# Optimization experiments

Measured on AMD Instinct MI355X. Metric: run time of the kernel, lower is better.

## Reference

```python
import jax, jax.numpy as jnp
import numpy as np

N = 20000      # nodes
E = 320000     # edges
IN = 300       # input_channel
HID = 100      # hidden_channel (= heads*out_channels with heads=1)
R = 50         # num_relations
B = 8          # num_bases (the 4th positional arg 'heads'=8 lands on num_bases in PyG RGATConv)
HEADS = 1
CLS = 3
Q = 64         # number of query (aspect) nodes
EPS = 1e-16


def setup_inputs() -> dict:
    key = jax.random.key(0)
    ks = jax.random.split(key, 16)
    x = jax.random.normal(ks[0], (N, IN), jnp.float32)
    edge_index = jax.random.randint(ks[1], (2, E), 0, N)
    edge_type = jax.random.randint(ks[2], (E,), 0, R)
    query_indices = jax.random.randint(ks[3], (Q,), 0, N)

    def w(k, shape, scale):
        return jax.random.normal(k, shape, jnp.float32) * scale

    comp1 = w(ks[4], (R, B), 0.3)
    basis1 = w(ks[5], (B, IN, HEADS * HID), 1.0 / np.sqrt(IN))
    q1 = w(ks[6], (HEADS * HID, HEADS), 0.1)
    k1 = w(ks[7], (HEADS * HID, HEADS), 0.1)
    b1 = jnp.zeros((HEADS * HID,), jnp.float32)
    comp2 = w(ks[8], (R, B), 0.3)
    basis2 = w(ks[9], (B, HID, HEADS * HID), 1.0 / np.sqrt(HID))
    q2 = w(ks[10], (HEADS * HID, HEADS), 0.1)
    k2 = w(ks[11], (HEADS * HID, HEADS), 0.1)
    b2 = jnp.zeros((HEADS * HID,), jnp.float32)
    Wl = w(ks[12], (CLS, HID), 1.0 / np.sqrt(HID))
    bl = jnp.zeros((CLS,), jnp.float32)
    return dict(x=x, edge_index=edge_index, edge_type=edge_type,
                query_indices=query_indices,
                comp1=comp1, basis1=basis1, q1=q1, k1=k1, b1=b1,
                comp2=comp2, basis2=basis2, q2=q2, k2=k2, b2=b2,
                Wl=Wl, bl=bl)


def segment_softmax(alpha, seg, num_segments):
    # numerically-stable softmax over edges grouped by destination node
    m = jax.ops.segment_max(alpha, seg, num_segments=num_segments)  # [N, H]
    e = jnp.exp(alpha - m[seg])
    s = jax.ops.segment_sum(e, seg, num_segments=num_segments)
    return e / (s[seg] + EPS)


def rgat_conv(x, edge_index, edge_type, comp, basis, q, k, b):
    # basis-decomposed per-relation weight: [R, in, H*out]
    W = jnp.einsum('rb,bio->rio', comp, basis)
    # transform every node under every relation once, then gather per edge
    xt = jnp.einsum('ni,rio->nro', x, W)          # [N, R, H*out]
    src, dst = edge_index[0], edge_index[1]        # j -> i (source_to_target)
    xi = xt[dst, edge_type]                        # [E, H*out]
    xj = xt[src, edge_type]                        # [E, H*out]
    qi = xi @ q                                    # [E, H]
    kj = xj @ k                                    # [E, H]
    alpha = jax.nn.leaky_relu(qi + kj, 0.2)        # additive self-attention
    alpha = segment_softmax(alpha, dst, N)         # across-relation softmax
    msg = xj.reshape(E, HEADS, HID) * alpha[:, :, None]
    out = jax.ops.segment_sum(msg, dst, num_segments=N)  # [N, H, out]
    return out.reshape(N, HEADS * HID) + b         # concat=True


def reference(x, edge_index, edge_type, query_indices,
              comp1, basis1, q1, k1, b1,
              comp2, basis2, q2, k2, b2, Wl, bl):
    h = jax.nn.relu(rgat_conv(x, edge_index, edge_type, comp1, basis1, q1, k1, b1))
    h = jax.nn.relu(rgat_conv(h, edge_index, edge_type, comp2, basis2, q2, k2, b2))
    pooled = h[query_indices].mean(axis=0)          # [HID]
    return pooled @ Wl.T + bl                       # [CLS]
```

## Files before the change

kernel.cpp:

```cpp
#include <hip/hip_runtime.h>
#include <math.h>

#define N_NODES 20000
#define E_EDGES 320000
#define IN_CH   300
#define HID     100
#define R_REL   50
#define NB      8
#define CLS     3
#define NQ      64
#define OUTW    800
#define ZW      100
#define SCAN_BLKS ((N_NODES + 255) / 256)

typedef unsigned short ushort_t;
typedef __attribute__((ext_vector_type(8))) short     short8;
typedef __attribute__((ext_vector_type(8))) unsigned short ushort8;
typedef __attribute__((ext_vector_type(4))) float     f32x4;
typedef __attribute__((ext_vector_type(2))) float     f32x2;

__device__ __forceinline__ ushort_t f2bf_rne(float f) {
    unsigned u = __float_as_uint(f);
    unsigned r = (u + 0x7fffu + ((u >> 16) & 1u)) >> 16;
    return (ushort_t)r;
}
__device__ __forceinline__ float bf2f(ushort_t u) {
    return __uint_as_float((unsigned)u << 16);
}

__global__ __launch_bounds__(256) void zero_deg2(int* __restrict__ dd,
                                                 int* __restrict__ ds) {
    int i = blockIdx.x * 256 + threadIdx.x;
    if (i < N_NODES) { dd[i] = 0; ds[i] = 0; }
}

__global__ __launch_bounds__(256) void hist2_kernel(
        const int* __restrict__ ei, int* __restrict__ dd,
        int* __restrict__ ds) {
    int e = blockIdx.x * 256 + threadIdx.x;
    if (e < E_EDGES) {
        atomicAdd(&dd[ei[E_EDGES + e]], 1);
        atomicAdd(&ds[ei[e]], 1);
    }
}

__global__ __launch_bounds__(256) void scan1_kernel(
        const int* __restrict__ deg, int* __restrict__ rowptr,
        int* __restrict__ bsum) {
    __shared__ int s[256];
    int tid = threadIdx.x;
    int idx = blockIdx.x * 256 + tid;
    int v = (idx < N_NODES) ? deg[idx] : 0;
    s[tid] = v; __syncthreads();
    #pragma unroll
    for (int off = 1; off < 256; off <<= 1) {
        int t = (tid >= off) ? s[tid - off] : 0;
        __syncthreads();
        s[tid] += t;
        __syncthreads();
    }
    if (idx < N_NODES) rowptr[idx] = s[tid] - v;
    if (tid == 255) bsum[blockIdx.x] = s[255];
}

__global__ __launch_bounds__(128) void scan2_kernel(int* __restrict__ bsum,
                                                    int* __restrict__ rowptr) {
    __shared__ int s[128];
    int tid = threadIdx.x;
    int v = (tid < SCAN_BLKS) ? bsum[tid] : 0;
    s[tid] = v; __syncthreads();
    #pragma unroll
    for (int off = 1; off < 128; off <<= 1) {
        int t = (tid >= off) ? s[tid - off] : 0;
        __syncthreads();
        s[tid] += t;
        __syncthreads();
    }
    if (tid < SCAN_BLKS) bsum[tid] = s[tid] - v;
    if (tid == 0) rowptr[N_NODES] = E_EDGES;
}

__global__ __launch_bounds__(256) void scan3_kernel(
        int* __restrict__ rowptr, const int* __restrict__ bsum,
        int* __restrict__ cursor) {
    int idx = blockIdx.x * 256 + threadIdx.x;
    if (idx < N_NODES) {
        int v = rowptr[idx] + bsum[blockIdx.x];
        rowptr[idx] = v;
        cursor[idx] = v;
    }
}

__global__ __launch_bounds__(256) void scatter_both(
        const int* __restrict__ ei, const int* __restrict__ et,
        int* __restrict__ cur_d, int* __restrict__ cur_s,
        int* __restrict__ skey, int* __restrict__ skey_s) {
    int e = blockIdx.x * 256 + threadIdx.x;
    if (e >= E_EDGES) return;
    int s = ei[e], d = ei[E_EDGES + e], rt = et[e];
    int p = atomicAdd(&cur_d[d], 1);
    skey[p] = (s << 6) | rt;
    int qp = atomicAdd(&cur_s[s], 1);
    skey_s[qp] = (p << 6) | rt;
}

__global__ __launch_bounds__(256) void split_bt_kernel(
        const float* __restrict__ basis, ushort_t* __restrict__ Bt,
        int K, int Kp) {
    int idx = blockIdx.x * 256 + threadIdx.x;
    if (idx >= OUTW * Kp) return;
    int n = idx / Kp, k = idx - n * Kp;
    int b = n / HID, o = n - b * HID;
    float v = 0.f;
    if (k < K) v = basis[((size_t)b * K + k) * HID + o];
    Bt[idx] = f2bf_rne(v);
}

#define BM 64
#define BN 160
__global__ __launch_bounds__(256) void gemm_mfma(
        const float* __restrict__ A, const ushort_t* __restrict__ Bt,
        ushort_t* __restrict__ xbh, int M, int K, int Kp, int do_relu) {
    __shared__ ushort_t As[BM][32];
    __shared__ ushort_t Bs[BN][32];
    int tid  = threadIdx.x;
    int lane = tid & 63, wave = tid >> 6;
    int ml = lane & 15, quad = lane >> 4;
    int wr = (wave >> 1) * 32, wc = (wave & 1) * 80;
    int row0 = blockIdx.y * BM, col0 = blockIdx.x * BN;
    int ra = tid >> 2, ch_a = tid & 3;
    int gr_a = row0 + ra;
    f32x4 acc[2][5] = {};
    int ksteps = Kp >> 5;
    for (int ks = 0; ks < ksteps; ks++) {
        int k0 = ks << 5;
        __syncthreads();
        {
            float vals[8];
            int kb = k0 + ch_a * 8;
            if (gr_a < M) {
                const float* ar = A + (size_t)gr_a * K;
                if (kb + 8 <= K) {
                    float4 f0 = *(const float4*)&ar[kb];
                    float4 f1 = *(const float4*)&ar[kb + 4];
                    vals[0]=f0.x; vals[1]=f0.y; vals[2]=f0.z; vals[3]=f0.w;
                    vals[4]=f1.x; vals[5]=f1.y; vals[6]=f1.z; vals[7]=f1.w;
                } else {
                    #pragma unroll
                    for (int i = 0; i < 8; i++)
                        vals[i] = (kb + i < K) ? ar[kb + i] : 0.f;
                }
                if (do_relu)
                    #pragma unroll
                    for (int i = 0; i < 8; i++) vals[i] = fmaxf(vals[i], 0.f);
            } else {
                #pragma unroll
                for (int i = 0; i < 8; i++) vals[i] = 0.f;
            }
            ushort8 hv;
            #pragma unroll
            for (int i = 0; i < 8; i++) hv[i] = f2bf_rne(vals[i]);
            int p1 = ch_a ^ (ra & 3);
            *(ushort8*)&As[ra][p1 * 8] = hv;
        }
        for (int t = tid; t < 640; t += 256) {
            int rb = t >> 2, ch = t & 3;
            int ph = ch ^ (rb & 3);
            ushort8 vh = *(const ushort8*)&Bt[(size_t)(col0 + rb) * Kp + k0 + ch * 8];
            *(ushort8*)&Bs[rb][ph * 8] = vh;
        }
        __syncthreads();
        int pq = quad ^ (ml & 3);
        short8 af[2], bf[5];
        #pragma unroll
        for (int mt = 0; mt < 2; mt++)
            af[mt] = *(const short8*)&As[wr + mt * 16 + ml][pq * 8];
        #pragma unroll
        for (int nt = 0; nt < 5; nt++)
            bf[nt] = *(const short8*)&Bs[wc + nt * 16 + ml][pq * 8];
        #pragma unroll
        for (int mt = 0; mt < 2; mt++)
            #pragma unroll
            for (int nt = 0; nt < 5; nt++)
                acc[mt][nt] = __builtin_amdgcn_mfma_f32_16x16x32_bf16(af[mt], bf[nt], acc[mt][nt], 0, 0, 0);
    }
    #pragma unroll
    for (int mt = 0; mt < 2; mt++) {
        #pragma unroll
        for (int nt = 0; nt < 5; nt++) {
            #pragma unroll
            for (int r = 0; r < 4; r++) {
                int grow = row0 + wr + mt * 16 + quad * 4 + r;
                if (grow < M)
                    xbh[(size_t)grow * OUTW + col0 + wc + nt * 16 + ml] =
                        f2bf_rne(acc[mt][nt][r]);
            }
        }
    }
}

__global__ __launch_bounds__(256) void qbkb_kernel(
        const float* __restrict__ basis, const float* __restrict__ q,
        const float* __restrict__ k, float* __restrict__ qb,
        float* __restrict__ kb, int K) {
    int idx = blockIdx.x * 256 + threadIdx.x;
    if (idx >= K * NB) return;
    int kk = idx >> 3, b = idx & 7;
    const float* br = basis + ((size_t)b * K + kk) * HID;
    float aq = 0.f, ak = 0.f;
    for (int o = 0; o < HID; o++) {
        float v = br[o];
        aq = fmaf(v, q[o], aq);
        ak = fmaf(v, k[o], ak);
    }
    qb[idx] = aq; kb[idx] = ak;
}

#define QKN 32
__global__ __launch_bounds__(256) void qk2_kernel(
        const float* __restrict__ x, const float* __restrict__ qb,
        const float* __restrict__ kb, float* __restrict__ xbq,
        float* __restrict__ xbk, int K, int do_relu) {
    __shared__ float sx[QKN][301];
    int tid = threadIdx.x;
    int n0 = blockIdx.x * QKN;
    for (int r = 0; r < QKN; r++) {
        int gn = n0 + r;
        if (gn >= N_NODES) break;
        const float* xr = x + (size_t)gn * K;
        for (int c = tid; c < K; c += 256) {
            float v = xr[c];
            if (do_relu) v = fmaxf(v, 0.f);
            sx[r][c] = v;
        }
    }
    __syncthreads();
    int n = tid >> 3, b = tid & 7;
    int gn = n0 + n;
    if (gn >= N_NODES) return;
    float aq = 0.f, ak = 0.f;
    for (int kk = 0; kk < K; kk++) {
        float v = sx[n][kk];
        aq = fmaf(v, qb[kk * NB + b], aq);
        ak = fmaf(v, kb[kk * NB + b], ak);
    }
    xbq[gn * NB + b] = aq;
    xbk[gn * NB + b] = ak;
}

__global__ __launch_bounds__(256) void compute_z(
        const int* __restrict__ rowptr_s, const int* __restrict__ skey_s,
        const float* __restrict__ comp, const ushort_t* __restrict__ xbh,
        ushort_t* __restrict__ Z) {
    int wave = threadIdx.x >> 6, lane = threadIdx.x & 63;
    int s = blockIdx.x * 4 + wave;
    if (s >= N_NODES) return;
    int beg = rowptr_s[s], end = rowptr_s[s + 1];
    if (beg == end) return;
    int o = lane * 2;
    f32x2 xrow[NB];
    if (lane < 50) {
        #pragma unroll
        for (int b = 0; b < NB; b++) {
            ushort2 xx = *(const ushort2*)&xbh[(size_t)s * OUTW + b * HID + o];
            xrow[b].x = bf2f(xx.x);
            xrow[b].y = bf2f(xx.y);
        }
    }
    for (int p = beg; p < end; p++) {
        int key = skey_s[p];
        int zpos = key >> 6, rt = key & 63;
        const float* cr = comp + rt * NB;
        if (lane < 50) {
            f32x2 z = {0.f, 0.f};
            #pragma unroll
            for (int b = 0; b < NB; b++) z += cr[b] * xrow[b];
            ushort2 zz;
            zz.x = f2bf_rne(z.x);
            zz.y = f2bf_rne(z.y);
            *(ushort2*)&Z[(size_t)zpos * ZW + o] = zz;
        }
    }
}

__global__ __launch_bounds__(256) void msg_soft(
        const int* __restrict__ rowptr, const int* __restrict__ skey,
        const float* __restrict__ comp, const ushort_t* __restrict__ Z,
        const float* __restrict__ xbq, const float* __restrict__ xbk,
        const float* __restrict__ bias, float* __restrict__ h) {
    int wave = threadIdx.x >> 6, lane = threadIdx.x & 63;
    int d = blockIdx.x * 4 + wave;
    if (d >= N_NODES) return;
    int beg = rowptr[d], end = rowptr[d + 1];

    float4 qd0 = *(const float4*)&xbq[d * NB];
    float4 qd1 = *(const float4*)&xbq[d * NB + 4];

    f32x2 acc = {0.f, 0.f};
    float m = -1e30f, l = 0.f;
    int o = lane * 2;

    for (int c0 = beg; c0 < end; c0 += 64) {
        int p = c0 + lane;
        bool valid = p < end;
        float a = -1e30f;
        if (valid) {
            int key = skey[p];
            int s = key >> 6, rt = key & 63;
            const float4 c0v = *(const float4*)&comp[rt * NB];
            const float4 c1v = *(const float4*)&comp[rt * NB + 4];
            const float4 k0v = *(const float4*)&xbk[s * NB];
            const float4 k1v = *(const float4*)&xbk[s * NB + 4];
            float qi = c0v.x*qd0.x + c0v.y*qd0.y + c0v.z*qd0.z + c0v.w*qd0.w
                     + c1v.x*qd1.x + c1v.y*qd1.y + c1v.z*qd1.z + c1v.w*qd1.w;
            float kj = c0v.x*k0v.x + c0v.y*k0v.y + c0v.z*k0v.z + c0v.w*k0v.w
                     + c1v.x*k1v.x + c1v.y*k1v.y + c1v.z*k1v.z + c1v.w*k1v.w;
            a = qi + kj;
            a = a > 0.f ? a : 0.2f * a;
        }
        float cm = a;
        #pragma unroll
        for (int off = 32; off; off >>= 1) cm = fmaxf(cm, __shfl_xor(cm, off));
        float M = fmaxf(m, cm);
        float scale = __expf(m - M);
        acc *= scale; l *= scale; m = M;
        float wgt = valid ? __expf(a - M) : 0.f;
        float cs = wgt;
        #pragma unroll
        for (int off = 32; off; off >>= 1) cs += __shfl_xor(cs, off);
        l += cs;
        int cnt = end - c0; if (cnt > 64) cnt = 64;
        for (int j = 0; j < cnt; j++) {
            float wj = __shfl(wgt, j);
            if (lane < 50) {
                ushort2 zz = *(const ushort2*)&Z[(size_t)(c0 + j) * ZW + o];
                f32x2 zv = {bf2f(zz.x), bf2f(zz.y)};
                acc += wj * zv;
            }
        }
    }
    if (lane < 50) {
        float inv = 1.f / (l + 1e-16f);
        f32x2 r;
        r.x = bias[o]     + acc.x * inv;
        r.y = bias[o + 1] + acc.y * inv;
        *(f32x2*)&h[(size_t)d * HID + o] = r;
    }
}

__global__ __launch_bounds__(128) void head_kernel(
        const float* __restrict__ h2, const int* __restrict__ qidx,
        const float* __restrict__ Wl, const float* __restrict__ bl,
        float* __restrict__ out) {
    __shared__ float pooled[HID];
    int tid = threadIdx.x;
    if (tid < HID) {
        float s = 0.f;
        for (int i = 0; i < NQ; i++)
            s += fmaxf(h2[(size_t)qidx[i] * HID + tid], 0.f);
        pooled[tid] = s * (1.0f / NQ);
    }
    __syncthreads();
    if (tid < CLS) {
        float s = bl[tid];
        for (int o = 0; o < HID; o++) s = fmaf(pooled[o], Wl[tid * HID + o], s);
        out[tid] = s;
    }
}

extern "C" void kernel_launch(void* const* d_in, const int* in_sizes, int n_in,
                              void* d_out, int out_size, void* d_ws, size_t ws_size,
                              hipStream_t stream) {
    const float* x      = (const float*)d_in[0];
    const int*   ei     = (const int*)  d_in[1];
    const int*   et     = (const int*)  d_in[2];
    const int*   qidx   = (const int*)  d_in[3];
    const float* comp1  = (const float*)d_in[4];
    const float* basis1 = (const float*)d_in[5];
    const float* q1     = (const float*)d_in[6];
    const float* k1     = (const float*)d_in[7];
    const float* b1     = (const float*)d_in[8];
    const float* comp2  = (const float*)d_in[9];
    const float* basis2 = (const float*)d_in[10];
    const float* q2     = (const float*)d_in[11];
    const float* k2     = (const float*)d_in[12];
    const float* b2     = (const float*)d_in[13];
    const float* Wl     = (const float*)d_in[14];
    const float* bl     = (const float*)d_in[15];
    float* out = (float*)d_out;

    const int KP1 = 320, KP2 = 128;

    char* w = (char*)d_ws;
    size_t off = 0;
    auto alloc = [&](size_t nbytes) {
        void* p = (void*)(w + off);
        off += ((nbytes + 255) / 256) * 256;
        return p;
    };
    ushort_t* xbh    = (ushort_t*)alloc((size_t)N_NODES * OUTW * 2);
    ushort_t* Z      = (ushort_t*)alloc((size_t)E_EDGES * ZW * 2);
    float*    h1     = (float*)alloc((size_t)N_NODES * HID * 4);
    float*    h2     = (float*)alloc((size_t)N_NODES * HID * 4);
    ushort_t* Bt     = (ushort_t*)alloc((size_t)OUTW * KP1 * 2);
    float*    xbq    = (float*)alloc((size_t)N_NODES * NB * 4);
    float*    xbk    = (float*)alloc((size_t)N_NODES * NB * 4);
    float*    qb     = (float*)alloc((size_t)KP1 * NB * 4);
    float*    kb     = (float*)alloc((size_t)KP1 * NB * 4);
    int*      deg_d  = (int*)alloc(N_NODES * 4);
    int*      deg_s  = (int*)alloc(N_NODES * 4);
    int*      rp_d   = (int*)alloc((N_NODES + 1) * 4);
    int*      rp_s   = (int*)alloc((N_NODES + 1) * 4);
    int*      cur_d  = (int*)alloc(N_NODES * 4);
    int*      cur_s  = (int*)alloc(N_NODES * 4);
    int*      bsum   = (int*)alloc(SCAN_BLKS * 4);
    int*      skey   = (int*)alloc(E_EDGES * 4);
    int*      skey_s = (int*)alloc(E_EDGES * 4);

    zero_deg2<<<SCAN_BLKS, 256, 0, stream>>>(deg_d, deg_s);
    hist2_kernel<<<(E_EDGES + 255) / 256, 256, 0, stream>>>(ei, deg_d, deg_s);
    scan1_kernel<<<SCAN_BLKS, 256, 0, stream>>>(deg_d, rp_d, bsum);
    scan2_kernel<<<1, 128, 0, stream>>>(bsum, rp_d);
    scan3_kernel<<<SCAN_BLKS, 256, 0, stream>>>(rp_d, bsum, cur_d);
    scan1_kernel<<<SCAN_BLKS, 256, 0, stream>>>(deg_s, rp_s, bsum);
    scan2_kernel<<<1, 128, 0, stream>>>(bsum, rp_s);
    scan3_kernel<<<SCAN_BLKS, 256, 0, stream>>>(rp_s, bsum, cur_s);
    scatter_both<<<(E_EDGES + 255) / 256, 256, 0, stream>>>(ei, et, cur_d, cur_s, skey, skey_s);

    auto layer = [&](const float* input, int K, int Kp, int relu_in,
                     const float* comp, const float* basis, const float* q,
                     const float* k, const float* bias, float* hout) {
        int nb = OUTW * Kp;
        split_bt_kernel<<<(nb + 255) / 256, 256, 0, stream>>>(basis, Bt, K, Kp);
        dim3 g(OUTW / BN, (N_NODES + BM - 1) / BM);
        gemm_mfma<<<g, 256, 0, stream>>>(input, Bt, xbh, N_NODES, K, Kp, relu_in);
        qbkb_kernel<<<(K * NB + 255) / 256, 256, 0, stream>>>(basis, q, k, qb, kb, K);
        qk2_kernel<<<(N_NODES + QKN - 1) / QKN, 256, 0, stream>>>(input, qb, kb, xbq, xbk, K, relu_in);
        compute_z<<<(N_NODES + 3) / 4, 256, 0, stream>>>(rp_s, skey_s, comp, xbh, Z);
        msg_soft<<<(N_NODES + 3) / 4, 256, 0, stream>>>(rp_d, skey, comp, Z, xbq, xbk, bias, hout);
    };

    layer(x,  IN_CH, KP1, 0, comp1, basis1, q1, k1, b1, h1);
    layer(h1, HID,   KP2, 1, comp2, basis2, q2, k2, b2, h2);
    head_kernel<<<1, 128, 0, stream>>>(h2, qidx, Wl, bl, out);
}
```

Baseline: 456.3 us.

## Keep full A row-block in LDS across column blocks; restage qk2 weights

The GEMM now loads each 64-row block of the input once into LDS as bf16 for the whole K range, then loops over all five 160-wide column blocks inside one workgroup. This removes the repeated fp32 A reads and conversions that happened once per column block, at the cost of about 42KB of LDS per block and fewer, longer workgroups. The qk2 kernel now caches the qb/kb projection tables in LDS and has each thread read its input row directly from global memory, replacing the per-block staging of input rows. ZW is also changed from 100 to 128.

```diff
diff --git a/kernel.cpp b/kernel.cpp
--- a/kernel.cpp
+++ b/kernel.cpp
@@ -10,7 +10,7 @@
 #define CLS     3
 #define NQ      64
 #define OUTW    800
-#define ZW      100
+#define ZW      128
 #define SCAN_BLKS ((N_NODES + 255) / 256)
 
 typedef unsigned short ushort_t;
@@ -118,28 +118,28 @@
 
 #define BM 64
 #define BN 160
+#define NCB (OUTW / BN)
 __global__ __launch_bounds__(256) void gemm_mfma(
         const float* __restrict__ A, const ushort_t* __restrict__ Bt,
         ushort_t* __restrict__ xbh, int M, int K, int Kp, int do_relu) {
-    __shared__ ushort_t As[BM][32];
+    __shared__ ushort_t As[64 * 328];
     __shared__ ushort_t Bs[BN][32];
     int tid  = threadIdx.x;
     int lane = tid & 63, wave = tid >> 6;
     int ml = lane & 15, quad = lane >> 4;
     int wr = (wave >> 1) * 32, wc = (wave & 1) * 80;
-    int row0 = blockIdx.y * BM, col0 = blockIdx.x * BN;
-    int ra = tid >> 2, ch_a = tid & 3;
-    int gr_a = row0 + ra;
-    f32x4 acc[2][5] = {};
+    int row0 = blockIdx.x * BM;
+    int SW = Kp + 8;
     int ksteps = Kp >> 5;
-    for (int ks = 0; ks < ksteps; ks++) {
-        int k0 = ks << 5;
-        __syncthreads();
-        {
+
+    {
+        int ra = tid >> 2;
+        int gr = row0 + ra;
+        const float* ar = A + (size_t)gr * K;
+        for (int c = (tid & 3); c * 8 < Kp; c += 4) {
+            int kb = c * 8;
             float vals[8];
-            int kb = k0 + ch_a * 8;
-            if (gr_a < M) {
-                const float* ar = A + (size_t)gr_a * K;
+            if (gr < M) {
                 if (kb + 8 <= K) {
                     float4 f0 = *(const float4*)&ar[kb];
                     float4 f1 = *(const float4*)&ar[kb + 4];
@@ -160,40 +160,48 @@
             ushort8 hv;
             #pragma unroll
             for (int i = 0; i < 8; i++) hv[i] = f2bf_rne(vals[i]);
-            int p1 = ch_a ^ (ra & 3);
-            *(ushort8*)&As[ra][p1 * 8] = hv;
-        }
-        for (int t = tid; t < 640; t += 256) {
-            int rb = t >> 2, ch = t & 3;
-            int ph = ch ^ (rb & 3);
-            ushort8 vh = *(const ushort8*)&Bt[(size_t)(col0 + rb) * Kp + k0 + ch * 8];
-            *(ushort8*)&Bs[rb][ph * 8] = vh;
-        }
-        __syncthreads();
-        int pq = quad ^ (ml & 3);
-        short8 af[2], bf[5];
+            *(ushort8*)&As[ra * SW + kb] = hv;
+        }
+    }
+
+    int pq = quad ^ (ml & 3);
+    for (int cb = 0; cb < NCB; cb++) {
+        int col0 = cb * BN;
+        f32x4 acc[2][5] = {};
+        for (int ks = 0; ks < ksteps; ks++) {
+            int k0 = ks << 5;
+            __syncthreads();
+            for (int t = tid; t < 640; t += 256) {
+                int rb = t >> 2, ch = t & 3;
+                int ph = ch ^ (rb & 3);
+                ushort8 vh = *(const ushort8*)&Bt[(size_t)(col0 + rb) * Kp + k0 + ch * 8];
+                *(ushort8*)&Bs[rb][ph * 8] = vh;
+            }
+            __syncthreads();
+            short8 af[2], bf[5];
+            #pragma unroll
+            for (int mt = 0; mt < 2; mt++)
+                af[mt] = *(const short8*)&As[(wr + mt * 16 + ml) * SW + k0 + quad * 8];
+            #pragma unroll
+            for (int nt = 0; nt < 5; nt++)
+                bf[nt] = *(const short8*)&Bs[wc + nt * 16 + ml][pq * 8];
+            #pragma unroll
+            for (int mt = 0; mt < 2; mt++)
+                #pragma unroll
+                for (int nt = 0; nt < 5; nt++)
+                    acc[mt][nt] = __builtin_amdgcn_mfma_f32_16x16x32_bf16(af[mt], bf[nt], acc[mt][nt], 0, 0, 0);
+        }
         #pragma unroll
-        for (int mt = 0; mt < 2; mt++)
-            af[mt] = *(const short8*)&As[wr + mt * 16 + ml][pq * 8];
-        #pragma unroll
-        for (int nt = 0; nt < 5; nt++)
-            bf[nt] = *(const short8*)&Bs[wc + nt * 16 + ml][pq * 8];
-        #pragma unroll
-        for (int mt = 0; mt < 2; mt++)
-            #pragma unroll
-            for (int nt = 0; nt < 5; nt++)
-                acc[mt][nt] = __builtin_amdgcn_mfma_f32_16x16x32_bf16(af[mt], bf[nt], acc[mt][nt], 0, 0, 0);
-    }
-    #pragma unroll
-    for (int mt = 0; mt < 2; mt++) {
-        #pragma unroll
-        for (int nt = 0; nt < 5; nt++) {
-            #pragma unroll
-            for (int r = 0; r < 4; r++) {
-                int grow = row0 + wr + mt * 16 + quad * 4 + r;
-                if (grow < M)
-                    xbh[(size_t)grow * OUTW + col0 + wc + nt * 16 + ml] =
-                        f2bf_rne(acc[mt][nt][r]);
+        for (int mt = 0; mt < 2; mt++) {
+            #pragma unroll
+            for (int nt = 0; nt < 5; nt++) {
+                #pragma unroll
+                for (int r = 0; r < 4; r++) {
+                    int grow = row0 + wr + mt * 16 + quad * 4 + r;
+                    if (grow < M)
+                        xbh[(size_t)grow * OUTW + col0 + wc + nt * 16 + ml] =
+                            f2bf_rne(acc[mt][nt][r]);
+                }
             }
         }
     }
@@ -216,36 +224,27 @@
     qb[idx] = aq; kb[idx] = ak;
 }
 
-#define QKN 32
 __global__ __launch_bounds__(256) void qk2_kernel(
         const float* __restrict__ x, const float* __restrict__ qb,
         const float* __restrict__ kb, float* __restrict__ xbq,
         float* __restrict__ xbk, int K, int do_relu) {
-    __shared__ float sx[QKN][301];
+    __shared__ float sqb[320 * NB], skb[320 * NB];
     int tid = threadIdx.x;
-    int n0 = blockIdx.x * QKN;
-    for (int r = 0; r < QKN; r++) {
-        int gn = n0 + r;
-        if (gn >= N_NODES) break;
-        const float* xr = x + (size_t)gn * K;
-        for (int c = tid; c < K; c += 256) {
-            float v = xr[c];
-            if (do_relu) v = fmaxf(v, 0.f);
-            sx[r][c] = v;
-        }
-    }
+    for (int i = tid; i < K * NB; i += 256) { sqb[i] = qb[i]; skb[i] = kb[i]; }
     __syncthreads();
-    int n = tid >> 3, b = tid & 7;
-    int gn = n0 + n;
-    if (gn >= N_NODES) return;
+    int idx = blockIdx.x * 256 + tid;
+    if (idx >= N_NODES * NB) return;
+    int n = idx >> 3, b = idx & 7;
+    const float* xr = x + (size_t)n * K;
     float aq = 0.f, ak = 0.f;
     for (int kk = 0; kk < K; kk++) {
-        float v = sx[n][kk];
-        aq = fmaf(v, qb[kk * NB + b], aq);
-        ak = fmaf(v, kb[kk * NB + b], ak);
-    }
-    xbq[gn * NB + b] = aq;
-    xbk[gn * NB + b] = ak;
+        float v = xr[kk];
+        if (do_relu) v = fmaxf(v, 0.f);
+        aq = fmaf(v, sqb[kk * NB + b], aq);
+        ak = fmaf(v, skb[kk * NB + b], ak);
+    }
+    xbq[idx] = aq;
+    xbk[idx] = ak;
 }
 
 __global__ __launch_bounds__(256) void compute_z(
@@ -432,10 +431,9 @@
                      const float* k, const float* bias, float* hout) {
         int nb = OUTW * Kp;
         split_bt_kernel<<<(nb + 255) / 256, 256, 0, stream>>>(basis, Bt, K, Kp);
-        dim3 g(OUTW / BN, (N_NODES + BM - 1) / BM);
-        gemm_mfma<<<g, 256, 0, stream>>>(input, Bt, xbh, N_NODES, K, Kp, relu_in);
+        gemm_mfma<<<(N_NODES + BM - 1) / BM, 256, 0, stream>>>(input, Bt, xbh, N_NODES, K, Kp, relu_in);
         qbkb_kernel<<<(K * NB + 255) / 256, 256, 0, stream>>>(basis, q, k, qb, kb, K);
-        qk2_kernel<<<(N_NODES + QKN - 1) / QKN, 256, 0, stream>>>(input, qb, kb, xbq, xbk, K, relu_in);
+        qk2_kernel<<<(N_NODES * NB + 255) / 256, 256, 0, stream>>>(input, qb, kb, xbq, xbk, K, relu_in);
         compute_z<<<(N_NODES + 3) / 4, 256, 0, stream>>>(rp_s, skey_s, comp, xbh, Z);
         msg_soft<<<(N_NODES + 3) / 4, 256, 0, stream>>>(rp_d, skey, comp, Z, xbq, xbk, bias, hout);
     };
```

Result: faster. 444.7 us (-2.5%).
